# Kernel optimization log

Measured on AMD Instinct MI355X. Metric: run time of the kernel, lower is better.

Reference implementation:

```python
import jax, jax.numpy as jnp
import numpy as np

BS, C_IN, J, T = 32, 3, 25, 512
DIM = 256
EPS = 1e-5


def _conv1x1(x, w, b=None):
    # x: [b, cin, j, t], w: [cout, cin]
    y = jnp.einsum('oc,bcjt->bojt', w, x)
    if b is not None:
        y = y + b[None, :, None, None]
    return y


def _bn(x, gamma, beta, axes):
    # training-mode batchnorm: batch stats, biased variance
    m = x.mean(axes, keepdims=True)
    v = x.var(axes, keepdims=True)
    shape = [1] * x.ndim
    shape[1] = -1
    return (x - m) / jnp.sqrt(v + EPS) * gamma.reshape(shape) + beta.reshape(shape)


def _embed_norm(x, bn_g, bn_b, w1, b1, w2, b2):
    bs, c, j, t = x.shape
    xn = _bn(x.reshape(bs, c * j, t), bn_g, bn_b, axes=(0, 2)).reshape(bs, c, j, t)
    h = jax.nn.relu(_conv1x1(xn, w1, b1))
    return jax.nn.relu(_conv1x1(h, w2, b2))


def _embed_nonorm(x, w1, b1, w2, b2):
    h = jax.nn.relu(_conv1x1(x, w1, b1))
    return jax.nn.relu(_conv1x1(h, w2, b2))


def _forward(Angle, dif, spa,
             je_bn_g, je_bn_b, je_w1, je_b1, je_w2, je_b2,
             df_bn_g, df_bn_b, df_w1, df_b1, df_w2, df_b2,
             sp_w1, sp_b1, sp_w2, sp_b2,
             g1_w, g1_b, g2_w, g2_b,
             gw, gw1, gw1_b, gbn_g, gbn_b):
    bs = Angle.shape[0]
    step = Angle.shape[3]
    a = _embed_norm(Angle, je_bn_g, je_bn_b, je_w1, je_b1, je_w2, je_b2)   # [b,64,J,T]
    d = _embed_norm(dif, df_bn_g, df_bn_b, df_w1, df_b1, df_w2, df_b2)    # [b,64,J,T]
    spa1 = _embed_nonorm(spa, sp_w1, sp_b1, sp_w2, sp_b2)                 # [1,64,J,1]
    spa1 = jnp.broadcast_to(spa1, (bs, spa1.shape[1], spa1.shape[2], step))
    inp = jnp.concatenate([a + d, spa1], axis=1)                          # [b,128,J,T]
    # compute_g_spa (regu1=regu2=0 -> no stochastic perturbation)
    q = _conv1x1(inp, g1_w, g1_b).transpose(0, 3, 2, 1)                   # [b,T,J,256]
    k = _conv1x1(inp, g2_w, g2_b).transpose(0, 3, 1, 2)                   # [b,T,256,J]
    g = jax.nn.softmax(jnp.matmul(q, k), axis=-1)                         # [b,T,J,J]
    # gcn_spa (GCNSma)
    xp = inp.transpose(0, 3, 2, 1)                                        # [b,T,J,128]
    xm = jnp.matmul(g, xp).transpose(0, 3, 2, 1)                          # [b,128,J,T]
    h = _conv1x1(xm, gw) + _conv1x1(inp, gw1, gw1_b)                      # [b,256,J,T]
    h = jax.nn.relu(_bn(h, gbn_g, gbn_b, axes=(0, 2, 3)))
    return h.max(axis=2, keepdims=True)                                   # [b,256,1,T]


def setup_inputs() -> dict:
    key = jax.random.key(0)
    ks = jax.random.split(key, 20)
    d4 = DIM // 4  # 64
    d2 = DIM // 2  # 128

    def w(k, o, c):
        return jax.random.normal(k, (o, c), dtype=jnp.float32) * np.float32(np.sqrt(2.0 / o))

    inp = {
        'Angle': jax.random.normal(ks[0], (BS, C_IN, J, T), dtype=jnp.float32),
        'dif': jax.random.normal(ks[1], (BS, C_IN, J, T), dtype=jnp.float32),
        'spa': jnp.eye(J, dtype=jnp.float32)[None, :, :, None],
        'je_bn_g': jnp.ones((C_IN * J,), jnp.float32), 'je_bn_b': jnp.zeros((C_IN * J,), jnp.float32),
        'je_w1': w(ks[2], 64, C_IN), 'je_b1': jnp.zeros((64,), jnp.float32),
        'je_w2': w(ks[3], d4, 64), 'je_b2': jnp.zeros((d4,), jnp.float32),
        'df_bn_g': jnp.ones((C_IN * J,), jnp.float32), 'df_bn_b': jnp.zeros((C_IN * J,), jnp.float32),
        'df_w1': w(ks[4], 64, C_IN), 'df_b1': jnp.zeros((64,), jnp.float32),
        'df_w2': w(ks[5], d4, 64), 'df_b2': jnp.zeros((d4,), jnp.float32),
        'sp_w1': w(ks[6], 64, J), 'sp_b1': jnp.zeros((64,), jnp.float32),
        'sp_w2': w(ks[7], d4, 64), 'sp_b2': jnp.zeros((d4,), jnp.float32),
        'g1_w': w(ks[8], DIM, d2), 'g1_b': jnp.zeros((DIM,), jnp.float32),
        'g2_w': w(ks[9], DIM, d2), 'g2_b': jnp.zeros((DIM,), jnp.float32),
        'gw': w(ks[10], DIM, d2),
        'gw1': w(ks[11], DIM, d2), 'gw1_b': jnp.zeros((DIM,), jnp.float32),
        'gbn_g': jnp.ones((DIM,), jnp.float32), 'gbn_b': jnp.zeros((DIM,), jnp.float32),
    }
    return inp


def reference(Angle, dif, spa,
              je_bn_g, je_bn_b, je_w1, je_b1, je_w2, je_b2,
              df_bn_g, df_bn_b, df_w1, df_b1, df_w2, df_b2,
              sp_w1, sp_b1, sp_w2, sp_b2,
              g1_w, g1_b, g2_w, g2_b,
              gw, gw1, gw1_b, gbn_g, gbn_b):
    return _forward(Angle, dif, spa,
                    je_bn_g, je_bn_b, je_w1, je_b1, je_w2, je_b2,
                    df_bn_g, df_bn_b, df_w1, df_b1, df_w2, df_b2,
                    sp_w1, sp_b1, sp_w2, sp_b2,
                    g1_w, g1_b, g2_w, g2_b,
                    gw, gw1, gw1_b, gbn_g, gbn_b)
```

## Files before the change

### kernel.cpp

```cpp
#include <hip/hip_runtime.h>
#include <hip/hip_bf16.h>

typedef __attribute__((ext_vector_type(8))) short short8;
typedef __attribute__((ext_vector_type(4))) float f32x4;
typedef __attribute__((ext_vector_type(4))) unsigned int u32x4;

__device__ __forceinline__ unsigned short f2b(float x){
  __hip_bfloat16 h = __float2bfloat16(x);
  union { __hip_bfloat16 h; unsigned short u; } cv;
  cv.h = h; return cv.u;
}

#define OFF_SBA    0
#define OFF_SBD    1024
#define OFF_SPA16  2048
#define OFF_W2AB   8704
#define OFF_W2DB   16896
#define OFF_BN2SB  25088
#define OFF_VVF    27136
#define OFF_ATB    27648
#define OFF_VVB    60416
#define OFF_WGB    64512
#define OFF_WG1B   130048
#define OFF_PART   195584
#define OFF_EXT    4389888
#define OFF_XBUF   21167104

__global__ void kprep1(const float* __restrict__ gw,  const float* __restrict__ gw1,
                       const float* __restrict__ je_w2, const float* __restrict__ df_w2,
                       const float* __restrict__ g2_w, const float* __restrict__ g1_b,
                       __hip_bfloat16* WG, __hip_bfloat16* WG1,
                       __hip_bfloat16* W2ab, __hip_bfloat16* W2db, float* vvf)
{
  int stride = gridDim.x * blockDim.x;
  for (int i = blockIdx.x*blockDim.x + threadIdx.x; i < 32768; i += stride){
    WG[i]  = __float2bfloat16(gw[i]);
    WG1[i] = __float2bfloat16(gw1[i]);
  }
  for (int i = blockIdx.x*blockDim.x + threadIdx.x; i < 4096; i += stride){
    W2ab[i] = __float2bfloat16(je_w2[i]);
    W2db[i] = __float2bfloat16(df_w2[i]);
  }
  for (int i = blockIdx.x*blockDim.x + threadIdx.x; i < 128; i += stride){
    float acc = 0.f;
    for (int o = 0; o < 256; ++o) acc += g2_w[o*128 + i] * g1_b[o];
    vvf[i] = acc;
  }
}

__global__ void kprep_at(const float* __restrict__ g1_w, const float* __restrict__ g2_w,
                         const float* __restrict__ vvf,
                         __hip_bfloat16* ATb, __hip_bfloat16* VVb)
{
  __shared__ float s1[64][16];
  __shared__ float s2[64][16];
  int tid = threadIdx.x;
  int bx = blockIdx.x & 7, by = blockIdx.x >> 3;
  if (blockIdx.x == 0){
    for (int i = tid; i < 2048; i += 256)
      VVb[i] = __float2bfloat16((i >> 7) == 0 ? vvf[i & 127] : 0.f);
  }
  int tc = tid & 15, tr = tid >> 4;
  float acc = 0.f;
  for (int och = 0; och < 4; ++och){
    for (int k = 0; k < 4; ++k){
      int idx = k*256 + tid;
      int ol = idx >> 4, cc = idx & 15;
      s1[ol][cc] = g1_w[(och*64 + ol)*128 + bx*16 + cc];
      s2[ol][cc] = g2_w[(och*64 + ol)*128 + by*16 + cc];
    }
    __syncthreads();
    for (int ol = 0; ol < 64; ++ol) acc += s2[ol][tr] * s1[ol][tc];
    __syncthreads();
  }
  ATb[(by*16 + tr)*128 + bx*16 + tc] = __float2bfloat16(acc);
}

__global__ void kspa(const float* __restrict__ w1, const float* __restrict__ b1,
                     const float* __restrict__ w2, const float* __restrict__ b2,
                     const float* __restrict__ spa, unsigned short* __restrict__ spa16)
{
  __shared__ float w1s[1600];
  __shared__ float sps[625];
  __shared__ float w2s[4096];
  __shared__ float r[64][26];
  int tid = threadIdx.x;
  for (int i = tid; i < 1600; i += 256) w1s[i] = w1[i];
  for (int i = tid; i < 625;  i += 256) sps[i] = spa[i];
  for (int i = tid; i < 4096; i += 256) w2s[i] = w2[i];
  __syncthreads();
  for (int i = tid; i < 1600; i += 256){
    int o = i/25, j = i%25;
    float acc = b1[o];
    for (int c = 0; c < 25; ++c) acc += w1s[o*25 + c] * sps[c*25 + j];
    r[o][j] = fmaxf(acc, 0.f);
  }
  __syncthreads();
  for (int i = tid; i < 2048; i += 256){
    int j = i >> 6, o2 = i & 63;
    float acc = 0.f;
    if (j < 25){
      acc = b2[o2];
      for (int c = 0; c < 64; ++c) acc += w2s[o2*64 + c] * r[c][j];
      acc = fmaxf(acc, 0.f);
    }
    spa16[j*64 + o2] = f2b(acc);
  }
}

__global__ void kbn1(const float* __restrict__ Angle, const float* __restrict__ dif,
                     const float* __restrict__ ga, const float* __restrict__ ba,
                     const float* __restrict__ gd, const float* __restrict__ bd,
                     float* sbA, float* sbD)
{
  __shared__ float red[256];
  __shared__ float red2[256];
  int blk = blockIdx.x;
  int which = blk / 75, cj = blk % 75;
  const float* x = which ? dif : Angle;
  int tid = threadIdx.x;
  float s = 0.f, q = 0.f;
  for (int i = tid; i < 16384; i += 256){
    int b = i >> 9, t = i & 511;
    float v = x[((size_t)b*75 + cj)*512 + t];
    s += v; q += v*v;
  }
  red[tid] = s; red2[tid] = q;
  __syncthreads();
  for (int off = 128; off > 0; off >>= 1){
    if (tid < off){ red[tid] += red[tid+off]; red2[tid] += red2[tid+off]; }
    __syncthreads();
  }
  if (tid == 0){
    float m = red[0] * (1.f/16384.f);
    float v = red2[0] * (1.f/16384.f) - m*m;
    float rstd = rsqrtf(v + 1e-5f);
    float g = (which ? gd : ga)[cj];
    float be = (which ? bd : ba)[cj];
    float sc = g * rstd;
    float* dst = which ? sbD : sbA;
    dst[cj*2]   = sc;
    dst[cj*2+1] = be - m*sc;
  }
}

__device__ __forceinline__ short8 ldfrag(const char* p){
  return *reinterpret_cast<const short8*>(p);
}
__device__ __forceinline__ short8 gfrag(const unsigned short* p){
  return *reinterpret_cast<const short8*>(p);
}

__global__ __launch_bounds__(256, 2) void kembed2(
    const float* __restrict__ Angle, const float* __restrict__ dif,
    const float* __restrict__ sbA, const float* __restrict__ sbD,
    const float* __restrict__ w1a, const float* __restrict__ b1a,
    const unsigned short* __restrict__ W2ab, const float* __restrict__ b2a,
    const float* __restrict__ w1d, const float* __restrict__ b1d,
    const unsigned short* __restrict__ W2db, const float* __restrict__ b2d,
    const unsigned short* __restrict__ spa16, unsigned short* __restrict__ X)
{
  __shared__ char lds[65536];
  char* hb = lds;
  char* ob = lds + 32768;
  const int tid = threadIdx.x;
  const int lane = tid & 63;
  const int w = tid >> 6;
  const int l15 = lane & 15;
  const int g = lane >> 4;
  const int tok0 = blockIdx.x * 4;
  const int b = tok0 >> 9;

  for (int idx = tid; idx < 512; idx += 256){
    int c = idx >> 3, e = idx & 7;
    float v;
    if (e < 3)       v = w1a[c*3 + e];
    else if (e == 3) v = b1a[c];
    else if (e < 7)  v = w1d[c*3 + (e - 4)];
    else             v = b1d[c];
    int bo = c*32 + ((e >= 4) ? 16 : 0) + (e & 3)*4;
    *(float*)(ob + (bo >> 7)*256 + (bo & 127)) = v;
  }
  __syncthreads();

  {
    int j = tid >> 3, sub = tid & 7, tl = sub >> 1, half = sub & 1;
    int row = tl*32 + j;
    int rsw = (row & 7) << 4;
    int t = (tok0 & 511) + tl;
    bool act = (j < 25);
    float xa[3], xd[3];
    if (act){
      #pragma unroll
      for (int cc = 0; cc < 3; ++cc){
        int cj = cc*25 + j;
        size_t off = ((size_t)(b*3+cc)*25 + j)*512 + t;
        xa[cc] = Angle[off]*sbA[2*cj] + sbA[2*cj+1];
        xd[cc] = dif[off]*sbD[2*cj] + sbD[2*cj+1];
      }
    }
    #pragma unroll
    for (int cblk = 0; cblk < 4; ++cblk){
      int base = half*32 + cblk*8;
      union { unsigned short us[8]; uint4 v; } pa, pd;
      #pragma unroll
      for (int k = 0; k < 8; ++k){
        int c = base + k;
        int bo = c*32;
        float4 fa = *(const float4*)(ob + (bo >> 7)*256 + (bo & 127));
        float4 fd = *(const float4*)(ob + ((bo+16) >> 7)*256 + ((bo+16) & 127));
        float ha = 0.f, hd = 0.f;
        if (act){
          ha = fmaxf(fa.w + fa.x*xa[0] + fa.y*xa[1] + fa.z*xa[2], 0.f);
          hd = fmaxf(fd.w + fd.x*xd[0] + fd.y*xd[1] + fd.z*xd[2], 0.f);
        }
        pa.us[k] = f2b(ha);
        pd.us[k] = f2b(hd);
      }
      *reinterpret_cast<uint4*>(hb + row*256 + ((2*base) ^ rsw)) = pa.v;
      *reinterpret_cast<uint4*>(hb + row*256 + ((128 + 2*base) ^ rsw)) = pd.v;
      uint4 ps = *(const uint4*)(spa16 + j*64 + base);
      *reinterpret_cast<uint4*>(ob + row*256 + ((128 + 2*base) ^ rsw)) = ps;
    }
  }
  __syncthreads();

  {
    short8 w2fa[4][2], w2fd[4][2];
    float ba4[4], bd4[4];
    #pragma unroll
    for (int nt = 0; nt < 4; ++nt){
      #pragma unroll
      for (int kk = 0; kk < 2; ++kk){
        w2fa[nt][kk] = gfrag(W2ab + (nt*16 + l15)*64 + kk*32 + g*8);
        w2fd[nt][kk] = gfrag(W2db + (nt*16 + l15)*64 + kk*32 + g*8);
      }
      ba4[nt] = b2a[nt*16 + l15];
      bd4[nt] = b2d[nt*16 + l15];
    }
    #pragma unroll
    for (int mt = 0; mt < 2; ++mt){
      int arow = w*32 + mt*16 + l15;
      f32x4 aA[4], aD[4];
      #pragma unroll
      for (int nt = 0; nt < 4; ++nt){
        f32x4 va = {ba4[nt], ba4[nt], ba4[nt], ba4[nt]};
        f32x4 vd = {bd4[nt], bd4[nt], bd4[nt], bd4[nt]};
        aA[nt] = va; aD[nt] = vd;
      }
      #pragma unroll
      for (int kk = 0; kk < 2; ++kk){
        int cba = (kk*64 + g*16) ^ ((l15 & 7) << 4);
        int cbd = ((128 + kk*64 + g*16)) ^ ((l15 & 7) << 4);
        short8 hA = ldfrag(hb + arow*256 + cba);
        short8 hD = ldfrag(hb + arow*256 + cbd);
        #pragma unroll
        for (int nt = 0; nt < 4; ++nt){
          aA[nt] = __builtin_amdgcn_mfma_f32_16x16x32_bf16(hA, w2fa[nt][kk], aA[nt], 0, 0, 0);
          aD[nt] = __builtin_amdgcn_mfma_f32_16x16x32_bf16(hD, w2fd[nt][kk], aD[nt], 0, 0, 0);
        }
      }
      #pragma unroll
      for (int nt = 0; nt < 4; ++nt)
        #pragma unroll
        for (int r = 0; r < 4; ++r){
          int row2 = w*32 + mt*16 + g*4 + r;
          float v = fmaxf(aA[nt][r], 0.f) + fmaxf(aD[nt][r], 0.f);
          if ((row2 & 31) >= 25) v = 0.f;
          int chb = (nt*16 + l15)*2;
          int addr = row2*256 + ((chb & ~15) ^ ((row2 & 7) << 4)) + (chb & 15);
          *(unsigned short*)(ob + addr) = f2b(v);
        }
    }
  }
  __syncthreads();

  {
    const uint4* ot = (const uint4*)ob;
    uint4* Xg = (uint4*)X;
    #pragma unroll
    for (int i2 = 0; i2 < 8; ++i2){
      int idx = i2*256 + tid;
      int trow = idx >> 4, off = idx & 15;
      Xg[((size_t)(tok0 + (trow >> 5)))*512 + (size_t)(trow & 31)*16 + off] = ot[idx];
    }
  }
}

#define FX0   0
#define FX1   8192
#define FY    16384
#define FZT   24576
#define FGT   45056
#define FWS   47616
#define FLDS  47744

__global__ __launch_bounds__(512, 2) void kfuse(
    const unsigned short* __restrict__ X,
    const unsigned short* __restrict__ ATb,
    const unsigned short* __restrict__ VVb,
    const unsigned short* __restrict__ WGb,
    const unsigned short* __restrict__ WG1b,
    const float* __restrict__ g_gw1b, const float* __restrict__ gbn_g,
    float* __restrict__ ext, float* __restrict__ partials)
{
  __shared__ char lds[FLDS];
  const int tid  = threadIdx.x;
  const int lane = tid & 63;
  const int w    = tid >> 6;
  const int l15  = lane & 15;
  const int g    = lane >> 4;
  const int swz  = (l15 & 7) << 4;

  short8 atf[4];
  #pragma unroll
  for (int kk = 0; kk < 4; ++kk)
    atf[kk] = gfrag(ATb + (w*16 + l15)*128 + kk*32 + g*8);

  float bh[2]; bool sg[2]; int oc_[2];
  #pragma unroll
  for (int n = 0; n < 2; ++n){
    int oc = w*32 + n*16 + l15;
    oc_[n] = oc;
    bh[n] = g_gw1b[oc];
    sg[n] = (gbn_g[oc] >= 0.f);
  }
  float rs[2] = {0.f,0.f}, rq[2] = {0.f,0.f};

  {
    const u32x4* tok = reinterpret_cast<const u32x4*>(X + (size_t)(blockIdx.x*8)*4096);
    u32x4 p = tok[tid];
    *reinterpret_cast<u32x4*>(lds + FX0 + tid*16) = p;
  }
  __syncthreads();

  int cur = 0;
  for (int it = 0; it < 8; ++it){
    const int token = blockIdx.x*8 + it;
    const char* Xc = lds + (cur ? FX1 : FX0);
    char* Xn = lds + (cur ? FX0 : FX1);

    int ntok = (it < 7) ? token + 1 : token;
    const u32x4* np = reinterpret_cast<const u32x4*>(X + (size_t)ntok*4096);
    u32x4 pfx = np[tid];

    short8 xc[4][2];
    #pragma unroll
    for (int kk = 0; kk < 4; ++kk){
      int cb = (kk*64 + g*16) ^ swz;
      xc[kk][0] = ldfrag(Xc + l15*256 + cb);
      xc[kk][1] = ldfrag(Xc + (16 + l15)*256 + cb);
    }

    {
      f32x4 ay0 = {0.f,0.f,0.f,0.f}, ay1 = {0.f,0.f,0.f,0.f};
      #pragma unroll
      for (int kk = 0; kk < 4; ++kk){
        ay0 = __builtin_amdgcn_mfma_f32_16x16x32_bf16(xc[kk][0], atf[kk], ay0, 0, 0, 0);
        ay1 = __builtin_amdgcn_mfma_f32_16x16x32_bf16(xc[kk][1], atf[kk], ay1, 0, 0, 0);
      }
      int col2 = (w*16 + l15)*2;
      #pragma unroll
      for (int r = 0; r < 4; ++r){
        int row0 = g*4 + r, row1 = 16 + g*4 + r;
        *(unsigned short*)(lds + FY + row0*256 + (col2 ^ ((row0&7)<<4))) = f2b(ay0[r]);
        *(unsigned short*)(lds + FY + row1*256 + (col2 ^ ((row1&7)<<4))) = f2b(ay1[r]);
      }
      if (w == 0){
        f32x4 aw0 = {0.f,0.f,0.f,0.f}, aw1 = {0.f,0.f,0.f,0.f};
        #pragma unroll
        for (int kk = 0; kk < 4; ++kk){
          short8 vfr = gfrag(VVb + l15*128 + kk*32 + g*8);
          aw0 = __builtin_amdgcn_mfma_f32_16x16x32_bf16(xc[kk][0], vfr, aw0, 0, 0, 0);
          aw1 = __builtin_amdgcn_mfma_f32_16x16x32_bf16(xc[kk][1], vfr, aw1, 0, 0, 0);
        }
        if (l15 == 0){
          #pragma unroll
          for (int r = 0; r < 4; ++r){
            *(float*)(lds + FWS + (g*4 + r)*4) = aw0[r];
            *(float*)(lds + FWS + (16 + g*4 + r)*4) = aw1[r];
          }
        }
      }
    }

    #pragma unroll
    for (int nt = 0; nt < 2; ++nt){
      int ocn = w*32 + nt*16 + l15;
      f32x4 az0 = {0.f,0.f,0.f,0.f}, az1 = {0.f,0.f,0.f,0.f};
      #pragma unroll
      for (int kk = 0; kk < 4; ++kk){
        short8 bz = gfrag(WGb + (size_t)ocn*128 + kk*32 + g*8);
        az0 = __builtin_amdgcn_mfma_f32_16x16x32_bf16(xc[kk][0], bz, az0, 0, 0, 0);
        az1 = __builtin_amdgcn_mfma_f32_16x16x32_bf16(xc[kk][1], bz, az1, 0, 0, 0);
      }
      union { unsigned short us[4]; uint2 v; } pk0, pk1;
      #pragma unroll
      for (int r = 0; r < 4; ++r){ pk0.us[r] = f2b(az0[r]); pk1.us[r] = f2b(az1[r]); }
      *(uint2*)(lds + FZT + ocn*80 + (g*4)*2)      = pk0.v;
      *(uint2*)(lds + FZT + ocn*80 + (16 + g*4)*2) = pk1.v;
    }
    __syncthreads();

    short8 g1f[2][4];
    #pragma unroll
    for (int nt = 0; nt < 2; ++nt)
      #pragma unroll
      for (int kk = 0; kk < 4; ++kk)
        g1f[nt][kk] = gfrag(WG1b + (size_t)(w*32 + nt*16 + l15)*128 + kk*32 + g*8);

    if (w < 2){
      const int Mt = w;
      f32x4 as0 = {0.f,0.f,0.f,0.f}, as1 = {0.f,0.f,0.f,0.f};
      #pragma unroll
      for (int kk = 0; kk < 4; ++kk){
        int cb = (kk*64 + g*16) ^ swz;
        short8 ya = ldfrag(lds + FY + (Mt*16 + l15)*256 + cb);
        as0 = __builtin_amdgcn_mfma_f32_16x16x32_bf16(ya, xc[kk][0], as0, 0, 0, 0);
        as1 = __builtin_amdgcn_mfma_f32_16x16x32_bf16(ya, xc[kk][1], as1, 0, 0, 0);
      }
      float wc0 = *(const float*)(lds + FWS + l15*4);
      float wc1 = *(const float*)(lds + FWS + 64 + l15*4);
      unsigned short* gt = (unsigned short*)(lds + FGT);
      #pragma unroll
      for (int r = 0; r < 4; ++r){
        int row = Mt*16 + g*4 + r;
        float v0 = as0[r] + wc0;
        float v1 = (l15 < 9) ? (as1[r] + wc1) : -3.0e38f;
        float m = fmaxf(v0, v1);
        m = fmaxf(m, __shfl_xor(m, 1));
        m = fmaxf(m, __shfl_xor(m, 2));
        m = fmaxf(m, __shfl_xor(m, 4));
        m = fmaxf(m, __shfl_xor(m, 8));
        float e0 = __expf(v0 - m);
        float e1 = (l15 < 9) ? __expf(v1 - m) : 0.f;
        float s = e0 + e1;
        s += __shfl_xor(s, 1);
        s += __shfl_xor(s, 2);
        s += __shfl_xor(s, 4);
        s += __shfl_xor(s, 8);
        float inv = 1.f / s;
        gt[row*40 + l15]      = f2b(e0 * inv);
        gt[row*40 + 16 + l15] = f2b(e1 * inv);
      }
    }

    *reinterpret_cast<u32x4*>(Xn + tid*16) = pfx;
    __syncthreads();

    f32x4 ah[2][2];
    #pragma unroll
    for (int nt = 0; nt < 2; ++nt){
      f32x4 b4 = {bh[nt], bh[nt], bh[nt], bh[nt]};
      ah[0][nt] = b4; ah[1][nt] = b4;
    }
    {
      short8 ga0 = ldfrag(lds + FGT + l15*80 + g*16);
      short8 ga1 = ldfrag(lds + FGT + (16 + l15)*80 + g*16);
      #pragma unroll
      for (int nt = 0; nt < 2; ++nt){
        short8 zb = ldfrag(lds + FZT + (w*32 + nt*16 + l15)*80 + g*16);
        ah[0][nt] = __builtin_amdgcn_mfma_f32_16x16x32_bf16(ga0, zb, ah[0][nt], 0, 0, 0);
        ah[1][nt] = __builtin_amdgcn_mfma_f32_16x16x32_bf16(ga1, zb, ah[1][nt], 0, 0, 0);
      }
    }
    #pragma unroll
    for (int kk = 0; kk < 4; ++kk)
      #pragma unroll
      for (int nt = 0; nt < 2; ++nt){
        ah[0][nt] = __builtin_amdgcn_mfma_f32_16x16x32_bf16(xc[kk][0], g1f[nt][kk], ah[0][nt], 0, 0, 0);
        ah[1][nt] = __builtin_amdgcn_mfma_f32_16x16x32_bf16(xc[kk][1], g1f[nt][kk], ah[1][nt], 0, 0, 0);
      }

    #pragma unroll
    for (int n = 0; n < 2; ++n){
      float e = sg[n] ? -3.0e38f : 3.0e38f;
      #pragma unroll
      for (int mt = 0; mt < 2; ++mt)
        #pragma unroll
        for (int r = 0; r < 4; ++r){
          int row = mt*16 + g*4 + r;
          if (row < 25){
            float v = ah[mt][n][r];
            rs[n] += v; rq[n] += v*v;
            e = sg[n] ? fmaxf(e, v) : fminf(e, v);
          }
        }
      float e2 = __shfl_xor(e, 16);
      e = sg[n] ? fmaxf(e, e2) : fminf(e, e2);
      e2 = __shfl_xor(e, 32);
      e = sg[n] ? fmaxf(e, e2) : fminf(e, e2);
      if (g == 0) ext[(size_t)token*256 + oc_[n]] = e;
    }
    cur ^= 1;
  }

  #pragma unroll
  for (int n = 0; n < 2; ++n){
    float s = rs[n], q = rq[n];
    s += __shfl_xor(s, 16); s += __shfl_xor(s, 32);
    q += __shfl_xor(q, 16); q += __shfl_xor(q, 32);
    if (g == 0){
      partials[(size_t)blockIdx.x*512 + oc_[n]]       = s;
      partials[(size_t)blockIdx.x*512 + 256 + oc_[n]] = q;
    }
  }
}

__global__ void kbn2(const float* __restrict__ partials,
                     const float* __restrict__ gg, const float* __restrict__ gb,
                     float* sb)
{
  __shared__ float red[256];
  __shared__ float red2[256];
  int oc = blockIdx.x, tid = threadIdx.x;
  float s = 0.f, q = 0.f;
  for (int i = tid; i < 2048; i += 256){
    s += partials[(size_t)i*512 + oc];
    q += partials[(size_t)i*512 + 256 + oc];
  }
  red[tid] = s; red2[tid] = q;
  __syncthreads();
  for (int off = 128; off > 0; off >>= 1){
    if (tid < off){ red[tid] += red[tid+off]; red2[tid] += red2[tid+off]; }
    __syncthreads();
  }
  if (tid == 0){
    float m = red[0] * (1.f/409600.f);
    float v = red2[0] * (1.f/409600.f) - m*m;
    float rstd = rsqrtf(v + 1e-5f);
    float sc = gg[oc]*rstd;
    sb[oc*2]   = sc;
    sb[oc*2+1] = gb[oc] - m*sc;
  }
}

__global__ void kpass2(const float* __restrict__ ext, const float* __restrict__ sb,
                       float* __restrict__ out)
{
  __shared__ float st[32][257];
  int b = blockIdx.x >> 4, tc = blockIdx.x & 15;
  int t0 = tc*32, tid = threadIdx.x;
  for (int i = tid; i < 32*256; i += 256){
    int tt = i >> 8, oc = i & 255;
    float v = ext[((size_t)(b*512) + t0 + tt)*256 + oc];
    st[tt][oc] = fmaxf(v*sb[oc*2] + sb[oc*2+1], 0.f);
  }
  __syncthreads();
  for (int i = tid; i < 32*256; i += 256){
    int oc = i >> 5, tt = i & 31;
    out[((size_t)(b*256) + oc)*512 + t0 + tt] = st[tt][oc];
  }
}

extern "C" void kernel_launch(void* const* d_in, const int* in_sizes, int n_in,
                              void* d_out, int out_size, void* d_ws, size_t ws_size,
                              hipStream_t stream)
{
  (void)in_sizes; (void)n_in; (void)out_size; (void)ws_size;
  const float* Angle = (const float*)d_in[0];
  const float* dif   = (const float*)d_in[1];
  const float* spa   = (const float*)d_in[2];
  const float* je_g  = (const float*)d_in[3];
  const float* je_b  = (const float*)d_in[4];
  const float* je_w1 = (const float*)d_in[5];
  const float* je_b1 = (const float*)d_in[6];
  const float* je_w2 = (const float*)d_in[7];
  const float* je_b2 = (const float*)d_in[8];
  const float* df_g  = (const float*)d_in[9];
  const float* df_b  = (const float*)d_in[10];
  const float* df_w1 = (const float*)d_in[11];
  const float* df_b1 = (const float*)d_in[12];
  const float* df_w2 = (const float*)d_in[13];
  const float* df_b2 = (const float*)d_in[14];
  const float* sp_w1 = (const float*)d_in[15];
  const float* sp_b1 = (const float*)d_in[16];
  const float* sp_w2 = (const float*)d_in[17];
  const float* sp_b2 = (const float*)d_in[18];
  const float* g1_w  = (const float*)d_in[19];
  const float* g1_b  = (const float*)d_in[20];
  const float* g2_w  = (const float*)d_in[21];
  const float* g2_b  = (const float*)d_in[22];
  const float* gw    = (const float*)d_in[23];
  const float* gw1   = (const float*)d_in[24];
  const float* gw1_b = (const float*)d_in[25];
  const float* gbn_g = (const float*)d_in[26];
  const float* gbn_b = (const float*)d_in[27];
  (void)g2_b;

  char* ws = (char*)d_ws;
  float* sbA     = (float*)(ws + OFF_SBA);
  float* sbD     = (float*)(ws + OFF_SBD);
  unsigned short* spa16 = (unsigned short*)(ws + OFF_SPA16);
  __hip_bfloat16* W2ab = (__hip_bfloat16*)(ws + OFF_W2AB);
  __hip_bfloat16* W2db = (__hip_bfloat16*)(ws + OFF_W2DB);
  float* bn2sb   = (float*)(ws + OFF_BN2SB);
  float* vvf     = (float*)(ws + OFF_VVF);
  __hip_bfloat16* ATb  = (__hip_bfloat16*)(ws + OFF_ATB);
  __hip_bfloat16* VVb  = (__hip_bfloat16*)(ws + OFF_VVB);
  __hip_bfloat16* WGb  = (__hip_bfloat16*)(ws + OFF_WGB);
  __hip_bfloat16* WG1b = (__hip_bfloat16*)(ws + OFF_WG1B);
  float* partials = (float*)(ws + OFF_PART);
  float* ext      = (float*)(ws + OFF_EXT);
  unsigned short* X = (unsigned short*)(ws + OFF_XBUF);

  kprep1<<<128, 256, 0, stream>>>(gw, gw1, je_w2, df_w2, g2_w, g1_b,
                                  WGb, WG1b, W2ab, W2db, vvf);
  kprep_at<<<64, 256, 0, stream>>>(g1_w, g2_w, vvf, ATb, VVb);
  kspa<<<1, 256, 0, stream>>>(sp_w1, sp_b1, sp_w2, sp_b2, spa, spa16);
  kbn1<<<150, 256, 0, stream>>>(Angle, dif, je_g, je_b, df_g, df_b, sbA, sbD);
  kembed2<<<4096, 256, 0, stream>>>(Angle, dif, sbA, sbD,
                                    je_w1, je_b1, (const unsigned short*)W2ab, je_b2,
                                    df_w1, df_b1, (const unsigned short*)W2db, df_b2,
                                    spa16, X);
  kfuse<<<2048, 512, 0, stream>>>(X,
                                  (const unsigned short*)ATb,
                                  (const unsigned short*)VVb,
                                  (const unsigned short*)WGb,
                                  (const unsigned short*)WG1b,
                                  gw1_b, gbn_g, ext, partials);
  kbn2<<<256, 256, 0, stream>>>(partials, gbn_g, gbn_b, bn2sb);
  kpass2<<<512, 256, 0, stream>>>(ext, bn2sb, (float*)d_out);
}
```

Before: 371.5 us.

## Merge prep kernels into one launch and overlap residual MFMAs with softmax

```diff
diff --git a/kernel.cpp b/kernel.cpp
--- a/kernel.cpp
+++ b/kernel.cpp
@@ -17,7 +17,6 @@
 #define OFF_W2AB   8704
 #define OFF_W2DB   16896
 #define OFF_BN2SB  25088
-#define OFF_VVF    27136
 #define OFF_ATB    27648
 #define OFF_VVB    60416
 #define OFF_WGB    64512
@@ -26,121 +25,119 @@
 #define OFF_EXT    4389888
 #define OFF_XBUF   21167104
 
-__global__ void kprep1(const float* __restrict__ gw,  const float* __restrict__ gw1,
-                       const float* __restrict__ je_w2, const float* __restrict__ df_w2,
-                       const float* __restrict__ g2_w, const float* __restrict__ g1_b,
-                       __hip_bfloat16* WG, __hip_bfloat16* WG1,
-                       __hip_bfloat16* W2ab, __hip_bfloat16* W2db, float* vvf)
+__global__ __launch_bounds__(256) void kpre(
+    const float* __restrict__ gw,  const float* __restrict__ gw1,
+    const float* __restrict__ je_w2, const float* __restrict__ df_w2,
+    const float* __restrict__ g1_w, const float* __restrict__ g2_w,
+    const float* __restrict__ g1_b,
+    const float* __restrict__ sp_w1, const float* __restrict__ sp_b1,
+    const float* __restrict__ sp_w2, const float* __restrict__ sp_b2,
+    const float* __restrict__ spa,
+    const float* __restrict__ Angle, const float* __restrict__ dif,
+    const float* __restrict__ je_g, const float* __restrict__ je_b,
+    const float* __restrict__ df_g, const float* __restrict__ df_b,
+    __hip_bfloat16* WG, __hip_bfloat16* WG1,
+    __hip_bfloat16* W2ab, __hip_bfloat16* W2db,
+    __hip_bfloat16* ATb, __hip_bfloat16* VVb,
+    unsigned short* spa16, float* sbA, float* sbD)
 {
-  int stride = gridDim.x * blockDim.x;
-  for (int i = blockIdx.x*blockDim.x + threadIdx.x; i < 32768; i += stride){
-    WG[i]  = __float2bfloat16(gw[i]);
-    WG1[i] = __float2bfloat16(gw1[i]);
-  }
-  for (int i = blockIdx.x*blockDim.x + threadIdx.x; i < 4096; i += stride){
-    W2ab[i] = __float2bfloat16(je_w2[i]);
-    W2db[i] = __float2bfloat16(df_w2[i]);
-  }
-  for (int i = blockIdx.x*blockDim.x + threadIdx.x; i < 128; i += stride){
+  __shared__ char buf[32768];
+  const int bid = blockIdx.x, tid = threadIdx.x;
+
+  if (bid < 128){
+    int base = bid*256 + tid, stride = 128*256;
+    for (int i = base; i < 32768; i += stride){
+      WG[i]  = __float2bfloat16(gw[i]);
+      WG1[i] = __float2bfloat16(gw1[i]);
+    }
+    for (int i = base; i < 4096; i += stride){
+      W2ab[i] = __float2bfloat16(je_w2[i]);
+      W2db[i] = __float2bfloat16(df_w2[i]);
+    }
+  } else if (bid == 128){
+    float* vv = (float*)buf;
+    if (tid < 128){
+      float acc = 0.f;
+      for (int o = 0; o < 256; ++o) acc += g2_w[o*128 + tid] * g1_b[o];
+      vv[tid] = acc;
+    }
+    __syncthreads();
+    for (int i = tid; i < 2048; i += 256)
+      VVb[i] = __float2bfloat16((i >> 7) == 0 ? vv[i & 127] : 0.f);
+  } else if (bid < 193){
+    float (*s1)[16] = (float(*)[16])buf;
+    float (*s2)[16] = (float(*)[16])(buf + 4096);
+    int bb = bid - 129;
+    int bx = bb & 7, by = bb >> 3;
+    int tc = tid & 15, tr = tid >> 4;
     float acc = 0.f;
-    for (int o = 0; o < 256; ++o) acc += g2_w[o*128 + i] * g1_b[o];
-    vvf[i] = acc;
-  }
-}
-
-__global__ void kprep_at(const float* __restrict__ g1_w, const float* __restrict__ g2_w,
-                         const float* __restrict__ vvf,
-                         __hip_bfloat16* ATb, __hip_bfloat16* VVb)
-{
-  __shared__ float s1[64][16];
-  __shared__ float s2[64][16];
-  int tid = threadIdx.x;
-  int bx = blockIdx.x & 7, by = blockIdx.x >> 3;
-  if (blockIdx.x == 0){
-    for (int i = tid; i < 2048; i += 256)
-      VVb[i] = __float2bfloat16((i >> 7) == 0 ? vvf[i & 127] : 0.f);
-  }
-  int tc = tid & 15, tr = tid >> 4;
-  float acc = 0.f;
-  for (int och = 0; och < 4; ++och){
-    for (int k = 0; k < 4; ++k){
-      int idx = k*256 + tid;
-      int ol = idx >> 4, cc = idx & 15;
-      s1[ol][cc] = g1_w[(och*64 + ol)*128 + bx*16 + cc];
-      s2[ol][cc] = g2_w[(och*64 + ol)*128 + by*16 + cc];
-    }
+    for (int och = 0; och < 4; ++och){
+      for (int k = 0; k < 4; ++k){
+        int idx = k*256 + tid;
+        int ol = idx >> 4, cc = idx & 15;
+        s1[ol][cc] = g1_w[(och*64 + ol)*128 + bx*16 + cc];
+        s2[ol][cc] = g2_w[(och*64 + ol)*128 + by*16 + cc];
+      }
+      __syncthreads();
+      for (int ol = 0; ol < 64; ++ol) acc += s2[ol][tr] * s1[ol][tc];
+      __syncthreads();
+    }
+    ATb[(by*16 + tr)*128 + bx*16 + tc] = __float2bfloat16(acc);
+  } else if (bid == 193){
+    float* w1s = (float*)buf;
+    float* sps = (float*)(buf + 6400);
+    float* w2s = (float*)(buf + 8960);
+    float (*r)[26] = (float(*)[26])(buf + 25344);
+    for (int i = tid; i < 1600; i += 256) w1s[i] = sp_w1[i];
+    for (int i = tid; i < 625;  i += 256) sps[i] = spa[i];
+    for (int i = tid; i < 4096; i += 256) w2s[i] = sp_w2[i];
     __syncthreads();
-    for (int ol = 0; ol < 64; ++ol) acc += s2[ol][tr] * s1[ol][tc];
+    for (int i = tid; i < 1600; i += 256){
+      int o = i/25, j = i%25;
+      float acc = sp_b1[o];
+      for (int c = 0; c < 25; ++c) acc += w1s[o*25 + c] * sps[c*25 + j];
+      r[o][j] = fmaxf(acc, 0.f);
+    }
     __syncthreads();
-  }
-  ATb[(by*16 + tr)*128 + bx*16 + tc] = __float2bfloat16(acc);
-}
-
-__global__ void kspa(const float* __restrict__ w1, const float* __restrict__ b1,
-                     const float* __restrict__ w2, const float* __restrict__ b2,
-                     const float* __restrict__ spa, unsigned short* __restrict__ spa16)
-{
-  __shared__ float w1s[1600];
-  __shared__ float sps[625];
-  __shared__ float w2s[4096];
-  __shared__ float r[64][26];
-  int tid = threadIdx.x;
-  for (int i = tid; i < 1600; i += 256) w1s[i] = w1[i];
-  for (int i = tid; i < 625;  i += 256) sps[i] = spa[i];
-  for (int i = tid; i < 4096; i += 256) w2s[i] = w2[i];
-  __syncthreads();
-  for (int i = tid; i < 1600; i += 256){
-    int o = i/25, j = i%25;
-    float acc = b1[o];
-    for (int c = 0; c < 25; ++c) acc += w1s[o*25 + c] * sps[c*25 + j];
-    r[o][j] = fmaxf(acc, 0.f);
-  }
-  __syncthreads();
-  for (int i = tid; i < 2048; i += 256){
-    int j = i >> 6, o2 = i & 63;
-    float acc = 0.f;
-    if (j < 25){
-      acc = b2[o2];
-      for (int c = 0; c < 64; ++c) acc += w2s[o2*64 + c] * r[c][j];
-      acc = fmaxf(acc, 0.f);
-    }
-    spa16[j*64 + o2] = f2b(acc);
-  }
-}
-
-__global__ void kbn1(const float* __restrict__ Angle, const float* __restrict__ dif,
-                     const float* __restrict__ ga, const float* __restrict__ ba,
-                     const float* __restrict__ gd, const float* __restrict__ bd,
-                     float* sbA, float* sbD)
-{
-  __shared__ float red[256];
-  __shared__ float red2[256];
-  int blk = blockIdx.x;
-  int which = blk / 75, cj = blk % 75;
-  const float* x = which ? dif : Angle;
-  int tid = threadIdx.x;
-  float s = 0.f, q = 0.f;
-  for (int i = tid; i < 16384; i += 256){
-    int b = i >> 9, t = i & 511;
-    float v = x[((size_t)b*75 + cj)*512 + t];
-    s += v; q += v*v;
-  }
-  red[tid] = s; red2[tid] = q;
-  __syncthreads();
-  for (int off = 128; off > 0; off >>= 1){
-    if (tid < off){ red[tid] += red[tid+off]; red2[tid] += red2[tid+off]; }
+    for (int i = tid; i < 2048; i += 256){
+      int j = i >> 6, o2 = i & 63;
+      float acc = 0.f;
+      if (j < 25){
+        acc = sp_b2[o2];
+        for (int c = 0; c < 64; ++c) acc += w2s[o2*64 + c] * r[c][j];
+        acc = fmaxf(acc, 0.f);
+      }
+      spa16[j*64 + o2] = f2b(acc);
+    }
+  } else {
+    float* red  = (float*)buf;
+    float* red2 = (float*)(buf + 1024);
+    int blk = bid - 194;
+    int which = blk / 75, cj = blk % 75;
+    const float* x = which ? dif : Angle;
+    float s = 0.f, q = 0.f;
+    for (int i = tid; i < 16384; i += 256){
+      int b = i >> 9, t = i & 511;
+      float v = x[((size_t)b*75 + cj)*512 + t];
+      s += v; q += v*v;
+    }
+    red[tid] = s; red2[tid] = q;
     __syncthreads();
-  }
-  if (tid == 0){
-    float m = red[0] * (1.f/16384.f);
-    float v = red2[0] * (1.f/16384.f) - m*m;
-    float rstd = rsqrtf(v + 1e-5f);
-    float g = (which ? gd : ga)[cj];
-    float be = (which ? bd : ba)[cj];
-    float sc = g * rstd;
-    float* dst = which ? sbD : sbA;
-    dst[cj*2]   = sc;
-    dst[cj*2+1] = be - m*sc;
+    for (int off = 128; off > 0; off >>= 1){
+      if (tid < off){ red[tid] += red[tid+off]; red2[tid] += red2[tid+off]; }
+      __syncthreads();
+    }
+    if (tid == 0){
+      float m = red[0] * (1.f/16384.f);
+      float v = red2[0] * (1.f/16384.f) - m*m;
+      float rstd = rsqrtf(v + 1e-5f);
+      float g = (which ? df_g : je_g)[cj];
+      float be = (which ? df_b : je_b)[cj];
+      float sc = g * rstd;
+      float* dst = which ? sbD : sbA;
+      dst[cj*2]   = sc;
+      dst[cj*2+1] = be - m*sc;
+    }
   }
 }
 
@@ -409,8 +406,16 @@
       for (int kk = 0; kk < 4; ++kk)
         g1f[nt][kk] = gfrag(WG1b + (size_t)(w*32 + nt*16 + l15)*128 + kk*32 + g*8);
 
+    f32x4 ah[2][2];
+    #pragma unroll
+    for (int nt = 0; nt < 2; ++nt){
+      f32x4 b4 = {bh[nt], bh[nt], bh[nt], bh[nt]};
+      ah[0][nt] = b4; ah[1][nt] = b4;
+    }
+
     if (w < 2){
       const int Mt = w;
+      __builtin_amdgcn_s_setprio(1);
       f32x4 as0 = {0.f,0.f,0.f,0.f}, as1 = {0.f,0.f,0.f,0.f};
       #pragma unroll
       for (int kk = 0; kk < 4; ++kk){
@@ -443,17 +448,27 @@
         gt[row*40 + l15]      = f2b(e0 * inv);
         gt[row*40 + 16 + l15] = f2b(e1 * inv);
       }
+      __builtin_amdgcn_s_setprio(0);
+      #pragma unroll
+      for (int kk = 0; kk < 4; ++kk)
+        #pragma unroll
+        for (int nt = 0; nt < 2; ++nt){
+          ah[0][nt] = __builtin_amdgcn_mfma_f32_16x16x32_bf16(xc[kk][0], g1f[nt][kk], ah[0][nt], 0, 0, 0);
+          ah[1][nt] = __builtin_amdgcn_mfma_f32_16x16x32_bf16(xc[kk][1], g1f[nt][kk], ah[1][nt], 0, 0, 0);
+        }
+    } else {
+      #pragma unroll
+      for (int kk = 0; kk < 4; ++kk)
+        #pragma unroll
+        for (int nt = 0; nt < 2; ++nt){
+          ah[0][nt] = __builtin_amdgcn_mfma_f32_16x16x32_bf16(xc[kk][0], g1f[nt][kk], ah[0][nt], 0, 0, 0);
+          ah[1][nt] = __builtin_amdgcn_mfma_f32_16x16x32_bf16(xc[kk][1], g1f[nt][kk], ah[1][nt], 0, 0, 0);
+        }
     }
 
     *reinterpret_cast<u32x4*>(Xn + tid*16) = pfx;
     __syncthreads();
 
-    f32x4 ah[2][2];
-    #pragma unroll
-    for (int nt = 0; nt < 2; ++nt){
-      f32x4 b4 = {bh[nt], bh[nt], bh[nt], bh[nt]};
-      ah[0][nt] = b4; ah[1][nt] = b4;
-    }
     {
       short8 ga0 = ldfrag(lds + FGT + l15*80 + g*16);
       short8 ga1 = ldfrag(lds + FGT + (16 + l15)*80 + g*16);
@@ -464,13 +479,6 @@
         ah[1][nt] = __builtin_amdgcn_mfma_f32_16x16x32_bf16(ga1, zb, ah[1][nt], 0, 0, 0);
       }
     }
-    #pragma unroll
-    for (int kk = 0; kk < 4; ++kk)
-      #pragma unroll
-      for (int nt = 0; nt < 2; ++nt){
-        ah[0][nt] = __builtin_amdgcn_mfma_f32_16x16x32_bf16(xc[kk][0], g1f[nt][kk], ah[0][nt], 0, 0, 0);
-        ah[1][nt] = __builtin_amdgcn_mfma_f32_16x16x32_bf16(xc[kk][1], g1f[nt][kk], ah[1][nt], 0, 0, 0);
-      }
 
     #pragma unroll
     for (int n = 0; n < 2; ++n){
@@ -595,7 +603,6 @@
   __hip_bfloat16* W2ab = (__hip_bfloat16*)(ws + OFF_W2AB);
   __hip_bfloat16* W2db = (__hip_bfloat16*)(ws + OFF_W2DB);
   float* bn2sb   = (float*)(ws + OFF_BN2SB);
-  float* vvf     = (float*)(ws + OFF_VVF);
   __hip_bfloat16* ATb  = (__hip_bfloat16*)(ws + OFF_ATB);
   __hip_bfloat16* VVb  = (__hip_bfloat16*)(ws + OFF_VVB);
   __hip_bfloat16* WGb  = (__hip_bfloat16*)(ws + OFF_WGB);
@@ -604,11 +611,11 @@
   float* ext      = (float*)(ws + OFF_EXT);
   unsigned short* X = (unsigned short*)(ws + OFF_XBUF);
 
-  kprep1<<<128, 256, 0, stream>>>(gw, gw1, je_w2, df_w2, g2_w, g1_b,
-                                  WGb, WG1b, W2ab, W2db, vvf);
-  kprep_at<<<64, 256, 0, stream>>>(g1_w, g2_w, vvf, ATb, VVb);
-  kspa<<<1, 256, 0, stream>>>(sp_w1, sp_b1, sp_w2, sp_b2, spa, spa16);
-  kbn1<<<150, 256, 0, stream>>>(Angle, dif, je_g, je_b, df_g, df_b, sbA, sbD);
+  kpre<<<344, 256, 0, stream>>>(gw, gw1, je_w2, df_w2, g1_w, g2_w, g1_b,
+                                sp_w1, sp_b1, sp_w2, sp_b2, spa,
+                                Angle, dif, je_g, je_b, df_g, df_b,
+                                WGb, WG1b, W2ab, W2db, ATb, VVb,
+                                spa16, sbA, sbD);
   kembed2<<<4096, 256, 0, stream>>>(Angle, dif, sbA, sbD,
                                     je_w1, je_b1, (const unsigned short*)W2ab, je_b2,
                                     df_w1, df_b1, (const unsigned short*)W2db, df_b2,
```

Result: faster. 333.9 us (-10.1%).
